# Performance work log

Hardware: AMD Instinct MI355X
Metric: run time of the kernel (lower is better)

Reference implementation:

```python
import jax, jax.numpy as jnp
import numpy as np

B, S, D, H = 32, 512, 512, 8  # note: source requires S == D due to swapped shape tuple in multi_head_attention
DK = D // H  # 64
FF = 200     # hard-coded FFN width in source
LN_EPS = 1e-5


def setup_inputs() -> dict:
    key = jax.random.key(0)
    ks = jax.random.split(key, 20)
    s = 0.02
    return {
        "x": jax.random.normal(ks[0], (B, S, D), dtype=jnp.float32),
        # per-head projections, stacked: torch Linear weight shape is [out, in] = [DK, D]
        "Wq": jax.random.normal(ks[1], (H, DK, D), dtype=jnp.float32) * s,
        "bq": jax.random.normal(ks[2], (H, DK), dtype=jnp.float32) * s,
        "Wk": jax.random.normal(ks[3], (H, DK, D), dtype=jnp.float32) * s,
        "bk": jax.random.normal(ks[4], (H, DK), dtype=jnp.float32) * s,
        "Wv": jax.random.normal(ks[5], (H, DK, D), dtype=jnp.float32) * s,
        "bv": jax.random.normal(ks[6], (H, DK), dtype=jnp.float32) * s,
        "Wo": jax.random.normal(ks[7], (D, D), dtype=jnp.float32) * s,
        "bo": jax.random.normal(ks[8], (D,), dtype=jnp.float32) * s,
        "W1": jax.random.normal(ks[9], (FF, D), dtype=jnp.float32) * s,
        "b1": jax.random.normal(ks[10], (FF,), dtype=jnp.float32) * s,
        "W2": jax.random.normal(ks[11], (FF, FF), dtype=jnp.float32) * s,
        "b2": jax.random.normal(ks[12], (FF,), dtype=jnp.float32) * s,
        "W3": jax.random.normal(ks[13], (D, FF), dtype=jnp.float32) * s,
        "b3": jax.random.normal(ks[14], (D,), dtype=jnp.float32) * s,
        # single SHARED LayerNorm over last two dims (S, D)
        "gamma": jnp.ones((S, D), dtype=jnp.float32),
        "beta": jnp.zeros((S, D), dtype=jnp.float32),
    }


def _layernorm2d(y, gamma, beta):
    # torch LayerNorm(normalized_shape=(S, D)): normalize over last two axes, biased variance
    m = jnp.mean(y, axis=(-2, -1), keepdims=True)
    v = jnp.mean(jnp.square(y - m), axis=(-2, -1), keepdims=True)
    return (y - m) * jax.lax.rsqrt(v + LN_EPS) * gamma + beta


def reference(x, Wq, bq, Wk, bk, Wv, bv, Wo, bo, W1, b1, W2, b2, W3, b3, gamma, beta):
    # --- multi-head attention (vectorized over the original per-head Python loop) ---
    q = jnp.einsum('bsd,hkd->bhsk', x, Wq) + bq[None, :, None, :]
    k = jnp.einsum('bsd,hkd->bhsk', x, Wk) + bk[None, :, None, :]
    v = jnp.einsum('bsd,hkd->bhsk', x, Wv) + bv[None, :, None, :]
    scores = jnp.einsum('bhsk,bhtk->bhst', q, k) / jnp.sqrt(jnp.float32(DK))
    attn = jax.nn.softmax(scores, axis=-1)
    heads = jnp.einsum('bhst,bhtk->bhsk', attn, v)          # [B,H,S,DK]
    concat = heads.transpose(0, 2, 1, 3).reshape(B, S, D)    # concat heads along feature dim
    y = jnp.einsum('bsd,ed->bse', concat, Wo) + bo + x       # output proj + residual
    # --- post-attention LayerNorm (shared params) ---
    y = _layernorm2d(y, gamma, beta)
    # --- feed-forward: D -> 200 -> 200 -> D, residual, LayerNorm (same shared LN) ---
    f = jax.nn.relu(jnp.einsum('bsd,fd->bsf', y, W1) + b1)
    f = jax.nn.relu(jnp.einsum('bsf,gf->bsg', f, W2) + b2)
    f = jnp.einsum('bsf,df->bsd', f, W3) + b3
    y = _layernorm2d(f + y, gamma, beta)
    # --- final LayerNorm (same shared LN again) ---
    return _layernorm2d(y, gamma, beta)
```

## Files before the change

### kernel.cpp

```cpp
#include <hip/hip_runtime.h>
#include <hip/hip_bf16.h>
#include <stdint.h>

#define B_  32
#define S_  512
#define D_  512
#define H_  8
#define DK_ 64
#define FF_ 200
#define FFP 256
#define M_  (B_*S_)
#define MSD ((size_t)B_*S_*D_)
#define NQKV 1536

typedef __hip_bfloat16 bf16;
typedef __attribute__((ext_vector_type(8))) short short8;
typedef __attribute__((ext_vector_type(4))) float f32x4;
typedef __attribute__((ext_vector_type(4))) unsigned short us4;

__device__ inline float b2f(bf16 v) { return __bfloat162float(v); }
__device__ inline bf16  f2b(float v){ return __float2bfloat16(v); }
__device__ inline unsigned short f2bu(float v) {
  union { bf16 h; unsigned short u; } cv; cv.h = __float2bfloat16(v); return cv.u;
}
__device__ inline float bu2f(unsigned short u) {
  union { unsigned short u; bf16 h; } cv; cv.u = u; return b2f(cv.h);
}
__device__ __forceinline__ void async16(const bf16* g, bf16* l) {
  __builtin_amdgcn_global_load_lds((const __attribute__((address_space(1))) void*)g,
                                   (__attribute__((address_space(3))) void*)l, 16, 0, 0);
}

__global__ void detect_kernel(const unsigned short* __restrict__ xu, int* __restrict__ flag,
                              float* __restrict__ stats) {
  __shared__ int mx[256];
  const int tid = threadIdx.x;
  if (tid < 192) stats[tid] = 0.f;
  int m = 0;
  for (int i = tid * 2; i < 8192; i += 512) {
    int e = (xu[i] >> 7) & 0xFF;
    m = m > e ? m : e;
  }
  mx[tid] = m;
  __syncthreads();
  for (int st = 128; st; st >>= 1) {
    if (tid < st) mx[tid] = mx[tid] > mx[tid + st] ? mx[tid] : mx[tid + st];
    __syncthreads();
  }
  if (tid == 0) *flag = (mx[0] >= 0xC0) ? 1 : 0;
}

__global__ __launch_bounds__(256) void cvt_x8(const void* __restrict__ in, bf16* __restrict__ out,
                                              const int* __restrict__ flag) {
  const bool f32in = (*flag != 0);
  size_t i = ((size_t)blockIdx.x * 256 + threadIdx.x) * 8;
  const size_t stride = (size_t)gridDim.x * 256 * 8;
  for (; i < MSD; i += stride) {
    if (f32in) {
      const float4 a = ((const float4*)in)[i/4];
      const float4 b = ((const float4*)in)[i/4 + 1];
      uint4 o; unsigned short* po = (unsigned short*)&o;
      po[0]=f2bu(a.x); po[1]=f2bu(a.y); po[2]=f2bu(a.z); po[3]=f2bu(a.w);
      po[4]=f2bu(b.x); po[5]=f2bu(b.y); po[6]=f2bu(b.z); po[7]=f2bu(b.w);
      *(uint4*)((unsigned short*)out + i) = o;
    } else {
      *(uint4*)((unsigned short*)out + i) = *(const uint4*)((const unsigned short*)in + i);
    }
  }
}

struct Seg { const void* src; void* dst; int srcRows, srcK, dstK, total; };
struct Segs { Seg s[16]; unsigned int isbf; };

__global__ __launch_bounds__(256) void cvt_all(Segs sg, const int* __restrict__ flag) {
  const bool f32in = (*flag != 0);
  const int seg = blockIdx.x & 15;
  const Seg sd = sg.s[seg];
  const int stride = (gridDim.x >> 4) * 256;
  const bool nopad = (sd.srcK == sd.dstK);
  for (int i = (blockIdx.x >> 4) * 256 + threadIdx.x; i < sd.total; i += stride) {
    int sidx; bool valid;
    if (nopad) { sidx = i; valid = (i < sd.srcRows * sd.srcK); }
    else {
      int r = i / sd.dstK, c = i - r * sd.dstK;
      valid = (r < sd.srcRows) && (c < sd.srcK);
      sidx = r * sd.srcK + c;
    }
    float v = 0.f;
    if (valid) v = f32in ? ((const float*)sd.src)[sidx] : b2f(((const bf16*)sd.src)[sidx]);
    if (sg.isbf & (1u << seg)) ((unsigned short*)sd.dst)[i] = f2bu(v);
    else                       ((float*)sd.dst)[i] = v;
  }
}

template<int MODE, int STATS>
__global__ __launch_bounds__(256) void gemm_mfma(
    const bf16* __restrict__ A, const bf16* __restrict__ W, const float* __restrict__ bias,
    const bf16* __restrict__ R, bf16* __restrict__ C, int M, int N, int K,
    float* __restrict__ stats)
{
  __shared__ __align__(16) char smem[18944];
  bf16*  As  = (bf16*)smem;
  bf16*  Bs  = (bf16*)(smem + 8192);
  float* Lf  = (float*)smem;
  float* red = (float*)(smem + 16896);

  const int tid  = threadIdx.x;
  const int bm   = blockIdx.x * 128;
  const int bn   = blockIdx.y * 128;
  const int w    = tid >> 6;
  const int lane = tid & 63;
  const int qd   = lane >> 4;
  const int ln   = lane & 15;
  const int wr   = (w >> 1) * 64;
  const int wc   = (w & 1) * 64;

  const int r0 = lane >> 2;
  const int ch = (lane & 3) * 8;
  const bf16* Ag0 = A + (size_t)(bm + w*16 + r0) * K + ch;
  const bf16* Ag1 = Ag0 + (size_t)64 * K;
  const bf16* Bg0 = W + (size_t)(bn + w*16 + r0) * K + ch;
  const bf16* Bg1 = Bg0 + (size_t)64 * K;
  bf16* Al0 = As + w*512 + lane*8;
  bf16* Al1 = Al0 + 2048;
  bf16* Bl0 = Bs + w*512 + lane*8;
  bf16* Bl1 = Bl0 + 2048;

  f32x4 acc[4][4] = {};

  for (int k0 = 0; k0 < K; k0 += 32) {
    async16(Ag0 + k0, Al0);
    async16(Ag1 + k0, Al1);
    async16(Bg0 + k0, Bl0);
    async16(Bg1 + k0, Bl1);
    __syncthreads();

    short8 af[4], bfr[4];
#pragma unroll
    for (int i = 0; i < 4; i++) af[i]  = *(const short8*)(As + (wr + i*16 + ln)*32 + qd*8);
#pragma unroll
    for (int j = 0; j < 4; j++) bfr[j] = *(const short8*)(Bs + (wc + j*16 + ln)*32 + qd*8);
#pragma unroll
    for (int i = 0; i < 4; i++)
#pragma unroll
      for (int j = 0; j < 4; j++)
        acc[i][j] = __builtin_amdgcn_mfma_f32_16x16x32_bf16(af[i], bfr[j], acc[i][j], 0, 0, 0);
    __syncthreads();
  }

  float s_acc = 0.f, ss_acc = 0.f;
  const int lrbase = (w >> 1)*16 + qd*4;
#pragma unroll
  for (int i = 0; i < 4; i++) {
#pragma unroll
    for (int j = 0; j < 4; j++) {
      const int col = wc + j*16 + ln;
#pragma unroll
      for (int rg = 0; rg < 4; rg++)
        Lf[(lrbase + rg)*132 + col] = acc[i][j][rg];
    }
    __syncthreads();
#pragma unroll
    for (int pz = 0; pz < 2; pz++) {
      const int q   = tid + pz*256;
      const int r   = q >> 4;
      const int nof = (q & 15)*8;
      const int m   = bm + (r >> 4)*64 + i*16 + (r & 15);
      const int n   = bn + nof;
      f32x4 v0 = *(const f32x4*)(Lf + r*132 + nof);
      f32x4 v1 = *(const f32x4*)(Lf + r*132 + nof + 4);
      f32x4 b0 = *(const f32x4*)(bias + n);
      f32x4 b1 = *(const f32x4*)(bias + n + 4);
      float vals[8];
#pragma unroll
      for (int e = 0; e < 4; e++) { vals[e] = v0[e] + b0[e]; vals[4+e] = v1[e] + b1[e]; }
      if (MODE == 1) {
#pragma unroll
        for (int e = 0; e < 8; e++) vals[e] = fmaxf(vals[e], 0.f);
      }
      if (MODE == 2) {
        const uint4 rv = *(const uint4*)((const unsigned short*)R + (size_t)m * N + n);
        const unsigned short* rp = (const unsigned short*)&rv;
#pragma unroll
        for (int e = 0; e < 8; e++) vals[e] += bu2f(rp[e]);
      }
      if (STATS) {
#pragma unroll
        for (int e = 0; e < 8; e++) { s_acc += vals[e]; ss_acc += vals[e]*vals[e]; }
      }
      uint4 o; unsigned short* op = (unsigned short*)&o;
#pragma unroll
      for (int e = 0; e < 8; e++) op[e] = f2bu(vals[e]);
      *(uint4*)((unsigned short*)C + (size_t)m * N + n) = o;
    }
    __syncthreads();
  }

  if (STATS) {
    red[tid] = s_acc; red[256 + tid] = ss_acc;
    __syncthreads();
    for (int st = 128; st; st >>= 1) {
      if (tid < st) { red[tid] += red[tid + st]; red[256 + tid] += red[256 + tid + st]; }
      __syncthreads();
    }
    if (tid == 0) {
      const int b = bm >> 9;
      atomicAdd(&stats[b*2],     red[0]);
      atomicAdd(&stats[b*2 + 1], red[256]);
    }
  }
}

__global__ __launch_bounds__(1024, 4) void attn_lds(const bf16* __restrict__ qkv,
                                                    bf16* __restrict__ cat)
{
  __shared__ bf16 Ks[2 * 512 * 32];
  __shared__ bf16 Vs[64 * 520];
  __shared__ bf16 pbuf[16][16][40];

  const int tid  = threadIdx.x;
  const int w    = tid >> 6;
  const int lane = tid & 63;
  const int qd   = lane >> 4;
  const int ln   = lane & 15;
  const int bh   = blockIdx.x;
  const int b    = bh >> 3, h = bh & 7;
  const bf16* base = qkv + (size_t)b * 512 * NQKV + h * 64;

  for (int c = tid; c < 4096; c += 1024) {
    int part = c & 3, key = (c >> 2) & 511, ks = c >> 11;
    async16(base + (size_t)key * NQKV + 512 + ks*32 + part*8, Ks + c*8);
  }
  for (int c = tid; c < 4096; c += 1024) {
    int dkg = c & 7, key = c >> 3;
    uint4 vv = *(const uint4*)(base + (size_t)key * NQKV + 1024 + dkg*8);
    const unsigned short* pv = (const unsigned short*)&vv;
#pragma unroll
    for (int j = 0; j < 8; j++)
      *(unsigned short*)&Vs[(dkg*8 + j)*520 + key] = pv[j];
  }
  short8 bq[2][2];
#pragma unroll
  for (int qt = 0; qt < 2; qt++)
#pragma unroll
    for (int ks = 0; ks < 2; ks++)
      bq[qt][ks] = *(const short8*)(base + (size_t)(w*32 + qt*16 + ln) * NQKV + ks*32 + qd*8);

  __syncthreads();

  bf16 (*pb)[40] = pbuf[w];
  f32x4 o[2][4] = {};
  float l[2] = {0.f, 0.f};

  for (int st = 0; st < 16; st++) {
    short8 ak[2][2];
#pragma unroll
    for (int kt = 0; kt < 2; kt++)
#pragma unroll
      for (int ks = 0; ks < 2; ks++)
        ak[kt][ks] = *(const short8*)(Ks + ks*16384 + (st*32 + kt*16 + ln)*32 + qd*8);
    f32x4 s[2][2] = {};
#pragma unroll
    for (int kt = 0; kt < 2; kt++)
#pragma unroll
      for (int qt = 0; qt < 2; qt++) {
        s[kt][qt] = __builtin_amdgcn_mfma_f32_16x16x32_bf16(ak[kt][0], bq[qt][0], s[kt][qt], 0, 0, 0);
        s[kt][qt] = __builtin_amdgcn_mfma_f32_16x16x32_bf16(ak[kt][1], bq[qt][1], s[kt][qt], 0, 0, 0);
      }
    float e[2][2][4];
#pragma unroll
    for (int kt = 0; kt < 2; kt++)
#pragma unroll
      for (int qt = 0; qt < 2; qt++)
#pragma unroll
        for (int rg = 0; rg < 4; rg++) {
          float ev = __expf(s[kt][qt][rg] * 0.125f);
          e[kt][qt][rg] = ev;
          l[qt] += ev;
        }
#pragma unroll
    for (int qt = 0; qt < 2; qt++) {
#pragma unroll
      for (int kt = 0; kt < 2; kt++) {
        uint2 pk;
        pk.x = (unsigned)f2bu(e[kt][qt][0]) | ((unsigned)f2bu(e[kt][qt][1]) << 16);
        pk.y = (unsigned)f2bu(e[kt][qt][2]) | ((unsigned)f2bu(e[kt][qt][3]) << 16);
        *(uint2*)&pb[ln][kt*16 + qd*4] = pk;
      }
      short8 ap = *(const short8*)&pb[ln][qd*8];
#pragma unroll
      for (int nt = 0; nt < 4; nt++) {
        short8 bv = *(const short8*)(Vs + (nt*16 + ln)*520 + st*32 + qd*8);
        o[qt][nt] = __builtin_amdgcn_mfma_f32_16x16x32_bf16(ap, bv, o[qt][nt], 0, 0, 0);
      }
    }
  }

#pragma unroll
  for (int qt = 0; qt < 2; qt++) {
    l[qt] += __shfl_xor(l[qt], 16);
    l[qt] += __shfl_xor(l[qt], 32);
  }
  float inv0 = 1.f / l[0], inv1 = 1.f / l[1];

  const size_t crow0 = (size_t)(b*S_ + w*32) * D_ + h*DK_;
#pragma unroll
  for (int qt = 0; qt < 2; qt++) {
#pragma unroll
    for (int rg = 0; rg < 4; rg++) {
      float ivv = __shfl(qt ? inv1 : inv0, qd*4 + rg);
      int r = qt*16 + qd*4 + rg;
      bf16* cp = cat + crow0 + (size_t)r * D_ + ln;
#pragma unroll
      for (int nt = 0; nt < 4; nt++) cp[nt*16] = f2b(o[qt][nt][rg] * ivv);
    }
  }
}

__global__ __launch_bounds__(256) void ln_b16_b16(const bf16* __restrict__ in,
    const float* __restrict__ stats, const bf16* __restrict__ gamma,
    const bf16* __restrict__ beta, bf16* __restrict__ out)
{
  const int b     = blockIdx.x & 31;
  const int slice = blockIdx.x >> 5;
  const float invN = 1.f / (float)(S_*D_);
  const float m    = stats[b*2] * invN;
  const float var  = stats[b*2+1] * invN - m*m;
  const float rstd = rsqrtf(var + 1e-5f);
  size_t v = (size_t)b * 65536 + slice * 4096 + threadIdx.x;
#pragma unroll 4
  for (int it = 0; it < 16; it++, v += 256) {
    us4 xi = *(const us4*)((const unsigned short*)in + v*4);
    size_t e = (v * 4) & (S_*D_ - 1);
    us4 g4 = *(const us4*)((const unsigned short*)gamma + e);
    us4 b4 = *(const us4*)((const unsigned short*)beta + e);
    us4 o;
    o[0] = f2bu((bu2f(xi[0]) - m) * rstd * bu2f(g4[0]) + bu2f(b4[0]));
    o[1] = f2bu((bu2f(xi[1]) - m) * rstd * bu2f(g4[1]) + bu2f(b4[1]));
    o[2] = f2bu((bu2f(xi[2]) - m) * rstd * bu2f(g4[2]) + bu2f(b4[2]));
    o[3] = f2bu((bu2f(xi[3]) - m) * rstd * bu2f(g4[3]) + bu2f(b4[3]));
    *(us4*)((unsigned short*)out + v*4) = o;
  }
}

__global__ __launch_bounds__(256) void ln_b16_b16_stats(const bf16* __restrict__ in,
    const float* __restrict__ stats, const bf16* __restrict__ gamma,
    const bf16* __restrict__ beta, bf16* __restrict__ out, float* __restrict__ stats3)
{
  __shared__ float red[512];
  const int b     = blockIdx.x & 31;
  const int slice = blockIdx.x >> 5;
  const float invN = 1.f / (float)(S_*D_);
  const float m    = stats[b*2] * invN;
  const float var  = stats[b*2+1] * invN - m*m;
  const float rstd = rsqrtf(var + 1e-5f);
  size_t v = (size_t)b * 65536 + slice * 4096 + threadIdx.x;
  float s_acc = 0.f, ss_acc = 0.f;
#pragma unroll 4
  for (int it = 0; it < 16; it++, v += 256) {
    us4 xi = *(const us4*)((const unsigned short*)in + v*4);
    size_t e = (v * 4) & (S_*D_ - 1);
    us4 g4 = *(const us4*)((const unsigned short*)gamma + e);
    us4 b4 = *(const us4*)((const unsigned short*)beta + e);
    float o0 = (bu2f(xi[0]) - m) * rstd * bu2f(g4[0]) + bu2f(b4[0]);
    float o1 = (bu2f(xi[1]) - m) * rstd * bu2f(g4[1]) + bu2f(b4[1]);
    float o2 = (bu2f(xi[2]) - m) * rstd * bu2f(g4[2]) + bu2f(b4[2]);
    float o3 = (bu2f(xi[3]) - m) * rstd * bu2f(g4[3]) + bu2f(b4[3]);
    us4 o;
    o[0] = f2bu(o0); o[1] = f2bu(o1); o[2] = f2bu(o2); o[3] = f2bu(o3);
    s_acc  += o0 + o1 + o2 + o3;
    ss_acc += o0*o0 + o1*o1 + o2*o2 + o3*o3;
    *(us4*)((unsigned short*)out + v*4) = o;
  }
  const int tid = threadIdx.x;
  red[tid] = s_acc; red[256 + tid] = ss_acc;
  __syncthreads();
  for (int st = 128; st; st >>= 1) {
    if (tid < st) { red[tid] += red[tid + st]; red[256 + tid] += red[256 + tid + st]; }
    __syncthreads();
  }
  if (tid == 0) {
    atomicAdd(&stats3[b*2],     red[0]);
    atomicAdd(&stats3[b*2 + 1], red[256]);
  }
}

__global__ __launch_bounds__(256) void ln_apply_out(const bf16* __restrict__ in,
    const float* __restrict__ stats, const bf16* __restrict__ gamma,
    const bf16* __restrict__ beta, void* __restrict__ out, const int* __restrict__ flag)
{
  const bool f32 = (*flag != 0);
  const int b     = blockIdx.x & 31;
  const int slice = blockIdx.x >> 5;
  const float invN = 1.f / (float)(S_*D_);
  const float m    = stats[b*2] * invN;
  const float var  = stats[b*2+1] * invN - m*m;
  const float rstd = rsqrtf(var + 1e-5f);
  size_t v = (size_t)b * 65536 + slice * 4096 + threadIdx.x;
#pragma unroll 4
  for (int it = 0; it < 16; it++, v += 256) {
    us4 xi = *(const us4*)((const unsigned short*)in + v*4);
    size_t e = (v * 4) & (S_*D_ - 1);
    us4 g4 = *(const us4*)((const unsigned short*)gamma + e);
    us4 b4 = *(const us4*)((const unsigned short*)beta + e);
    float4 o;
    o.x = (bu2f(xi[0]) - m) * rstd * bu2f(g4[0]) + bu2f(b4[0]);
    o.y = (bu2f(xi[1]) - m) * rstd * bu2f(g4[1]) + bu2f(b4[1]);
    o.z = (bu2f(xi[2]) - m) * rstd * bu2f(g4[2]) + bu2f(b4[2]);
    o.w = (bu2f(xi[3]) - m) * rstd * bu2f(g4[3]) + bu2f(b4[3]);
    if (f32) ((float4*)out)[v] = o;
    else {
      us4 ob;
      ob[0] = f2bu(o.x); ob[1] = f2bu(o.y); ob[2] = f2bu(o.z); ob[3] = f2bu(o.w);
      *(us4*)((unsigned short*)out + v*4) = ob;
    }
  }
}

extern "C" void kernel_launch(void* const* d_in, const int* in_sizes, int n_in,
                              void* d_out, int out_size, void* d_ws, size_t ws_size,
                              hipStream_t stream)
{
  char* p = (char*)d_ws;
  auto alloc_b = [&](size_t elems) { void* r = p; p += elems * 2; return (bf16*)r; };
  auto alloc_f = [&](size_t elems) {
    p = (char*)(((uintptr_t)p + 15) & ~(uintptr_t)15); void* r = p; p += elems * 4; return (float*)r;
  };

  bf16* xb   = alloc_b(MSD);
  bf16* qkv  = alloc_b(3 * MSD);
  bf16* catb = alloc_b(MSD);
  bf16* wqkv = alloc_b(3 * 512 * 512);
  bf16* wo   = alloc_b(512 * 512);
  bf16* w1p  = alloc_b((size_t)FFP * 512);
  bf16* w2p  = alloc_b((size_t)FFP * FFP);
  bf16* w3p  = alloc_b((size_t)512 * FFP);
  bf16* gm   = alloc_b((size_t)S_ * D_);
  bf16* bt   = alloc_b((size_t)S_ * D_);
  float* bqkv= alloc_f(3 * 512);
  float* bo  = alloc_f(512);
  float* b1p = alloc_f(FFP);
  float* b2p = alloc_f(FFP);
  float* b3  = alloc_f(512);
  float* stats = alloc_f(192);
  int*   flag  = (int*)alloc_f(16);
  if ((size_t)(p - (char*)d_ws) > ws_size) return;

  bf16* y1b = qkv;
  bf16* f1  = qkv + MSD;
  bf16* f2  = qkv + MSD + (size_t)M_ * FFP;
  bf16* yA  = qkv + 2 * MSD;
  bf16* yB  = catb;
  bf16* y2b = yA;
  float* st1 = stats, *st2 = stats + 64, *st3 = stats + 128;

  detect_kernel<<<1, 256, 0, stream>>>((const unsigned short*)d_in[0], flag, stats);
  cvt_x8<<<2048, 256, 0, stream>>>(d_in[0], xb, flag);

  Segs sg;
  sg.s[0]  = { d_in[1],  wqkv,               512, 512, 512, 512*512 };
  sg.s[1]  = { d_in[3],  wqkv + 512*512,     512, 512, 512, 512*512 };
  sg.s[2]  = { d_in[5],  wqkv + 2*512*512,   512, 512, 512, 512*512 };
  sg.s[3]  = { d_in[7],  wo,                 512, 512, 512, 512*512 };
  sg.s[4]  = { d_in[9],  w1p,                FF_, 512, 512, FFP*512 };
  sg.s[5]  = { d_in[11], w2p,                FF_, FF_, FFP, FFP*FFP };
  sg.s[6]  = { d_in[13], w3p,                512, FF_, FFP, 512*FFP };
  sg.s[7]  = { d_in[2],  bqkv,               1, 512, 512, 512 };
  sg.s[8]  = { d_in[4],  bqkv + 512,         1, 512, 512, 512 };
  sg.s[9]  = { d_in[6],  bqkv + 1024,        1, 512, 512, 512 };
  sg.s[10] = { d_in[8],  bo,                 1, 512, 512, 512 };
  sg.s[11] = { d_in[10], b1p,                1, FF_, FFP, FFP };
  sg.s[12] = { d_in[12], b2p,                1, FF_, FFP, FFP };
  sg.s[13] = { d_in[14], b3,                 1, 512, 512, 512 };
  sg.s[14] = { d_in[15], gm,                 1, S_*D_, S_*D_, S_*D_ };
  sg.s[15] = { d_in[16], bt,                 1, S_*D_, S_*D_, S_*D_ };
  sg.isbf = 0xC07F;
  cvt_all<<<1024, 256, 0, stream>>>(sg, flag);

  dim3 blk(256);

  gemm_mfma<0, 0><<<dim3(M_/128, NQKV/128), blk, 0, stream>>>(
      xb, wqkv, bqkv, nullptr, qkv, M_, NQKV, 512, nullptr);

  attn_lds<<<B_*H_, 1024, 0, stream>>>(qkv, catb);

  gemm_mfma<2, 1><<<dim3(M_/128, 4), blk, 0, stream>>>(
      catb, wo, bo, xb, yA, M_, 512, 512, st1);

  ln_b16_b16<<<512, blk, 0, stream>>>(yA, st1, gm, bt, y1b);

  gemm_mfma<1, 0><<<dim3(M_/128, 2), blk, 0, stream>>>(
      y1b, w1p, b1p, nullptr, f1, M_, FFP, 512, nullptr);
  gemm_mfma<1, 0><<<dim3(M_/128, 2), blk, 0, stream>>>(
      f1, w2p, b2p, nullptr, f2, M_, FFP, FFP, nullptr);
  gemm_mfma<2, 1><<<dim3(M_/128, 4), blk, 0, stream>>>(
      f2, w3p, b3, y1b, yB, M_, 512, FFP, st2);

  ln_b16_b16_stats<<<512, blk, 0, stream>>>(yB, st2, gm, bt, y2b, st3);
  ln_apply_out<<<512, blk, 0, stream>>>(y2b, st3, gm, bt, d_out, flag);
}
```

Baseline: 301.6 us.

## Double-buffer GEMM LDS tiles and reorder grids for row-block locality

The GEMM main loop now keeps two LDS buffers and issues the async loads for the next K-tile before computing the current one. It waits with explicit vmcnt counts and raw s_barrier instead of two full __syncthreads per iteration, aiming to hide global load latency. The grid is also transposed so consecutive blocks share the same A row-block across N tiles, and the LayerNorm kernels map consecutive blocks to the same batch, both to improve cache locality. LDS use grows to 32 KB per block, which may reduce occupancy, and the epilogue scratch still aliases the buffers, which relies on the final barrier.

```diff
diff --git a/kernel.cpp b/kernel.cpp
--- a/kernel.cpp
+++ b/kernel.cpp
@@ -99,15 +99,15 @@
     const bf16* __restrict__ R, bf16* __restrict__ C, int M, int N, int K,
     float* __restrict__ stats)
 {
-  __shared__ __align__(16) char smem[18944];
+  __shared__ __align__(16) char smem[32768];
   bf16*  As  = (bf16*)smem;
-  bf16*  Bs  = (bf16*)(smem + 8192);
+  bf16*  Bs  = (bf16*)(smem + 16384);
   float* Lf  = (float*)smem;
   float* red = (float*)(smem + 16896);
 
   const int tid  = threadIdx.x;
-  const int bm   = blockIdx.x * 128;
-  const int bn   = blockIdx.y * 128;
+  const int bm   = blockIdx.y * 128;
+  const int bn   = blockIdx.x * 128;
   const int w    = tid >> 6;
   const int lane = tid & 63;
   const int qd   = lane >> 4;
@@ -121,31 +121,44 @@
   const bf16* Ag1 = Ag0 + (size_t)64 * K;
   const bf16* Bg0 = W + (size_t)(bn + w*16 + r0) * K + ch;
   const bf16* Bg1 = Bg0 + (size_t)64 * K;
-  bf16* Al0 = As + w*512 + lane*8;
-  bf16* Al1 = Al0 + 2048;
-  bf16* Bl0 = Bs + w*512 + lane*8;
-  bf16* Bl1 = Bl0 + 2048;
+  const int lo = w*512 + lane*8;
 
   f32x4 acc[4][4] = {};
-
-  for (int k0 = 0; k0 < K; k0 += 32) {
-    async16(Ag0 + k0, Al0);
-    async16(Ag1 + k0, Al1);
-    async16(Bg0 + k0, Bl0);
-    async16(Bg1 + k0, Bl1);
-    __syncthreads();
+  const int nt = K >> 5;
+
+  async16(Ag0, As + lo);
+  async16(Ag1, As + lo + 2048);
+  async16(Bg0, Bs + lo);
+  async16(Bg1, Bs + lo + 2048);
+
+  for (int t = 0; t < nt; t++) {
+    const int cur = (t & 1) << 12;
+    if (t + 1 < nt) {
+      const int nxt = ((t + 1) & 1) << 12;
+      const int k0  = (t + 1) << 5;
+      async16(Ag0 + k0, As + nxt + lo);
+      async16(Ag1 + k0, As + nxt + lo + 2048);
+      async16(Bg0 + k0, Bs + nxt + lo);
+      async16(Bg1 + k0, Bs + nxt + lo + 2048);
+      asm volatile("s_waitcnt vmcnt(4)" ::: "memory");
+    } else {
+      asm volatile("s_waitcnt vmcnt(0)" ::: "memory");
+    }
+    __builtin_amdgcn_s_barrier();
 
     short8 af[4], bfr[4];
 #pragma unroll
-    for (int i = 0; i < 4; i++) af[i]  = *(const short8*)(As + (wr + i*16 + ln)*32 + qd*8);
-#pragma unroll
-    for (int j = 0; j < 4; j++) bfr[j] = *(const short8*)(Bs + (wc + j*16 + ln)*32 + qd*8);
+    for (int i = 0; i < 4; i++) af[i]  = *(const short8*)(As + cur + (wr + i*16 + ln)*32 + qd*8);
+#pragma unroll
+    for (int j = 0; j < 4; j++) bfr[j] = *(const short8*)(Bs + cur + (wc + j*16 + ln)*32 + qd*8);
 #pragma unroll
     for (int i = 0; i < 4; i++)
 #pragma unroll
       for (int j = 0; j < 4; j++)
         acc[i][j] = __builtin_amdgcn_mfma_f32_16x16x32_bf16(af[i], bfr[j], acc[i][j], 0, 0, 0);
-    __syncthreads();
+
+    asm volatile("" ::: "memory");
+    __builtin_amdgcn_s_barrier();
   }
 
   float s_acc = 0.f, ss_acc = 0.f;
@@ -321,13 +334,12 @@
     const float* __restrict__ stats, const bf16* __restrict__ gamma,
     const bf16* __restrict__ beta, bf16* __restrict__ out)
 {
-  const int b     = blockIdx.x & 31;
-  const int slice = blockIdx.x >> 5;
+  const int b = blockIdx.x >> 4;
   const float invN = 1.f / (float)(S_*D_);
   const float m    = stats[b*2] * invN;
   const float var  = stats[b*2+1] * invN - m*m;
   const float rstd = rsqrtf(var + 1e-5f);
-  size_t v = (size_t)b * 65536 + slice * 4096 + threadIdx.x;
+  size_t v = (size_t)b * 65536 + (blockIdx.x & 15) * 4096 + threadIdx.x;
 #pragma unroll 4
   for (int it = 0; it < 16; it++, v += 256) {
     us4 xi = *(const us4*)((const unsigned short*)in + v*4);
@@ -348,13 +360,12 @@
     const bf16* __restrict__ beta, bf16* __restrict__ out, float* __restrict__ stats3)
 {
   __shared__ float red[512];
-  const int b     = blockIdx.x & 31;
-  const int slice = blockIdx.x >> 5;
+  const int b = blockIdx.x >> 4;
   const float invN = 1.f / (float)(S_*D_);
   const float m    = stats[b*2] * invN;
   const float var  = stats[b*2+1] * invN - m*m;
   const float rstd = rsqrtf(var + 1e-5f);
-  size_t v = (size_t)b * 65536 + slice * 4096 + threadIdx.x;
+  size_t v = (size_t)b * 65536 + (blockIdx.x & 15) * 4096 + threadIdx.x;
   float s_acc = 0.f, ss_acc = 0.f;
 #pragma unroll 4
   for (int it = 0; it < 16; it++, v += 256) {
@@ -390,13 +401,12 @@
     const bf16* __restrict__ beta, void* __restrict__ out, const int* __restrict__ flag)
 {
   const bool f32 = (*flag != 0);
-  const int b     = blockIdx.x & 31;
-  const int slice = blockIdx.x >> 5;
+  const int b = blockIdx.x >> 4;
   const float invN = 1.f / (float)(S_*D_);
   const float m    = stats[b*2] * invN;
   const float var  = stats[b*2+1] * invN - m*m;
   const float rstd = rsqrtf(var + 1e-5f);
-  size_t v = (size_t)b * 65536 + slice * 4096 + threadIdx.x;
+  size_t v = (size_t)b * 65536 + (blockIdx.x & 15) * 4096 + threadIdx.x;
 #pragma unroll 4
   for (int it = 0; it < 16; it++, v += 256) {
     us4 xi = *(const us4*)((const unsigned short*)in + v*4);
@@ -479,21 +489,21 @@
 
   dim3 blk(256);
 
-  gemm_mfma<0, 0><<<dim3(M_/128, NQKV/128), blk, 0, stream>>>(
+  gemm_mfma<0, 0><<<dim3(NQKV/128, M_/128), blk, 0, stream>>>(
       xb, wqkv, bqkv, nullptr, qkv, M_, NQKV, 512, nullptr);
 
   attn_lds<<<B_*H_, 1024, 0, stream>>>(qkv, catb);
 
-  gemm_mfma<2, 1><<<dim3(M_/128, 4), blk, 0, stream>>>(
+  gemm_mfma<2, 1><<<dim3(4, M_/128), blk, 0, stream>>>(
       catb, wo, bo, xb, yA, M_, 512, 512, st1);
 
   ln_b16_b16<<<512, blk, 0, stream>>>(yA, st1, gm, bt, y1b);
 
-  gemm_mfma<1, 0><<<dim3(M_/128, 2), blk, 0, stream>>>(
+  gemm_mfma<1, 0><<<dim3(2, M_/128), blk, 0, stream>>>(
       y1b, w1p, b1p, nullptr, f1, M_, FFP, 512, nullptr);
-  gemm_mfma<1, 0><<<dim3(M_/128, 2), blk, 0, stream>>>(
+  gemm_mfma<1, 0><<<dim3(2, M_/128), blk, 0, stream>>>(
       f1, w2p, b2p, nullptr, f2, M_, FFP, FFP, nullptr);
-  gemm_mfma<2, 1><<<dim3(M_/128, 4), blk, 0, stream>>>(
+  gemm_mfma<2, 1><<<dim3(4, M_/128), blk, 0, stream>>>(
       f2, w3p, b3, y1b, yB, M_, 512, FFP, st2);
 
   ln_b16_b16_stats<<<512, blk, 0, stream>>>(yB, st2, gm, bt, y2b, st3);
```

Result: faster. 291.4 us (-3.4%).
